# Kernel optimization log

Measured on AMD Instinct MI355X. Metric: run time of the kernel, lower is better.

Reference implementation:

```python
import jax, jax.numpy as jnp
import numpy as np

B, S, D = 2, 2048, 1024
H, DH = 16, 64
E, K, FH = 8, 2, 4096
AUX_W = 0.01
EPS = 1e-6


def setup_inputs() -> dict:
    key = jax.random.key(0)
    ks = jax.random.split(key, 20)
    init = lambda k, shape: (jax.random.normal(k, shape, dtype=jnp.float32) * 0.02)
    return {
        'x': jax.random.normal(ks[0], (B, S, D), dtype=jnp.float32),
        'ln1_s': jnp.ones((D,), jnp.float32), 'ln1_b': jnp.zeros((D,), jnp.float32),
        'Wq': init(ks[1], (D, H * DH)), 'bq': jnp.zeros((H * DH,), jnp.float32),
        'Wk': init(ks[2], (D, H * DH)), 'bk': jnp.zeros((H * DH,), jnp.float32),
        'Wv': init(ks[3], (D, H * DH)), 'bv': jnp.zeros((H * DH,), jnp.float32),
        'Wo': init(ks[4], (H * DH, D)), 'bo': jnp.zeros((D,), jnp.float32),
        'ln2_s': jnp.ones((D,), jnp.float32), 'ln2_b': jnp.zeros((D,), jnp.float32),
        'Wg': init(ks[5], (D, E)), 'bg': jnp.zeros((E,), jnp.float32),
        'W1': init(ks[6], (E, D, FH)), 'b1': jnp.zeros((E, FH), jnp.float32),
        'W2': init(ks[7], (E, FH, D)), 'b2': jnp.zeros((E, D), jnp.float32),
    }


def _layer_norm(x, scale, bias):
    mu = jnp.mean(x, axis=-1, keepdims=True)
    var = jnp.mean(jnp.square(x - mu), axis=-1, keepdims=True)
    return (x - mu) * jax.lax.rsqrt(var + EPS) * scale + bias


def _causal_attn(x, Wq, bq, Wk, bk, Wv, bv, Wo, bo):
    b, s, _ = x.shape
    q = (x @ Wq + bq).reshape(b, s, H, DH)
    k = (x @ Wk + bk).reshape(b, s, H, DH)
    v = (x @ Wv + bv).reshape(b, s, H, DH)
    scores = jnp.einsum('bqhd,bkhd->bhqk', q, k) / jnp.sqrt(jnp.float32(DH))
    causal = jnp.tril(jnp.ones((s, s), dtype=bool))
    scores = jnp.where(causal, scores, jnp.finfo(scores.dtype).min)
    attn = jax.nn.softmax(scores, axis=-1)
    out = jnp.einsum('bhqk,bkhd->bqhd', attn, v).reshape(b, s, H * DH)
    return out @ Wo + bo


def _moe(x, Wg, bg, W1, b1, W2, b2):
    # x: (B,S,D) -> tokens (T,D)
    T = x.shape[0] * x.shape[1]
    xf = x.reshape(T, D)
    logits = xf @ Wg + bg                      # (T,E)
    probs = jax.nn.softmax(logits, axis=-1)
    topv, topi = jax.lax.top_k(probs, K)       # (T,K)
    topv = topv / jnp.sum(topv, axis=-1, keepdims=True)
    combine = jnp.zeros((T, E), xf.dtype).at[jnp.arange(T)[:, None], topi].set(topv)
    out = jnp.zeros((T, D), xf.dtype)
    for e in range(E):  # fixed small expert loop
        h = jax.nn.gelu(xf @ W1[e] + b1[e])
        out = out + combine[:, e:e + 1] * (h @ W2[e] + b2[e])
    # load-balance aux loss
    frac = jnp.mean((combine > 0).astype(jnp.float32), axis=0)
    pmean = jnp.mean(probs, axis=0)
    aux = AUX_W * E * jnp.sum(frac * pmean)
    return out.reshape(x.shape), aux


def reference(x, ln1_s, ln1_b, Wq, bq, Wk, bk, Wv, bv, Wo, bo,
              ln2_s, ln2_b, Wg, bg, W1, b1, W2, b2):
    working = x
    attn_in = _layer_norm(working, ln1_s, ln1_b)
    attn_out = _causal_attn(attn_in, Wq, bq, Wk, bk, Wv, bv, Wo, bo)
    working = working + attn_out
    ffn_in = _layer_norm(working, ln2_s, ln2_b)
    ffn_out, aux = _moe(ffn_in, Wg, bg, W1, b1, W2, b2)
    output = working + ffn_out
    return output, aux
```

## Files before the change

### kernel.cpp

```cpp
#include <hip/hip_runtime.h>
#include <hip/hip_bf16.h>
#include <math.h>

#define Bb 2
#define Ss 2048
#define Dd 1024
#define Hh 16
#define DH 64
#define Ee 8
#define FH 4096
#define Tt (Bb*Ss)

typedef __attribute__((ext_vector_type(8))) short short8;
typedef __attribute__((ext_vector_type(4))) short short4v;
typedef __attribute__((ext_vector_type(4))) float float4v;

#define AS 40

static __device__ inline short f2bf(float f) {
    __hip_bfloat16 h = __float2bfloat16(f);
    return *reinterpret_cast<short*>(&h);
}

__global__ __launch_bounds__(256) void ln_kernel(const float* __restrict__ x,
                                                 const float* __restrict__ sc,
                                                 const float* __restrict__ bi,
                                                 __hip_bfloat16* __restrict__ y) {
    int t = blockIdx.x, tid = threadIdx.x;
    const float* xr = x + (size_t)t * Dd;
    float s1 = 0.f, s2 = 0.f;
    for (int d = tid; d < Dd; d += 256) { float v = xr[d]; s1 += v; s2 += v * v; }
    __shared__ float r1[256], r2[256];
    r1[tid] = s1; r2[tid] = s2; __syncthreads();
    for (int off = 128; off > 0; off >>= 1) {
        if (tid < off) { r1[tid] += r1[tid + off]; r2[tid] += r2[tid + off]; }
        __syncthreads();
    }
    float mu = r1[0] * (1.f / Dd);
    float var = r2[0] * (1.f / Dd) - mu * mu;
    float rstd = rsqrtf(var + 1e-6f);
    __hip_bfloat16* yr = y + (size_t)t * Dd;
    for (int d = tid; d < Dd; d += 256) {
        float v = xr[d];
        yr[d] = __float2bfloat16((v - mu) * rstd * sc[d] + bi[d]);
    }
}

__global__ __launch_bounds__(256) void transpose_qkvo(
    const float* W0, const float* W1, const float* W2, const float* W3,
    __hip_bfloat16* T0, __hip_bfloat16* T1, __hip_bfloat16* T2, __hip_bfloat16* T3) {
    int z = blockIdx.z;
    const float* W = (z == 0) ? W0 : (z == 1) ? W1 : (z == 2) ? W2 : W3;
    __hip_bfloat16* Wt = (z == 0) ? T0 : (z == 1) ? T1 : (z == 2) ? T2 : T3;
    __shared__ float tile[32][33];
    int k0 = blockIdx.y * 32, n0 = blockIdx.x * 32;
    int tx = threadIdx.x & 31, ty = threadIdx.x >> 5;
    #pragma unroll
    for (int p = 0; p < 4; p++)
        tile[ty + p * 8][tx] = W[(size_t)(k0 + ty + p * 8) * Dd + n0 + tx];
    __syncthreads();
    #pragma unroll
    for (int p = 0; p < 4; p++)
        Wt[(size_t)(n0 + ty + p * 8) * Dd + k0 + tx] = __float2bfloat16(tile[tx][ty + p * 8]);
}

__global__ __launch_bounds__(256) void transpose_we(const float* __restrict__ W,
                                                    __hip_bfloat16* __restrict__ Wt,
                                                    int Kd, int N) {
    int e = blockIdx.z;
    W  += (size_t)e * Kd * N;
    Wt += (size_t)e * Kd * N;
    __shared__ float tile[32][33];
    int k0 = blockIdx.y * 32, n0 = blockIdx.x * 32;
    int tx = threadIdx.x & 31, ty = threadIdx.x >> 5;
    #pragma unroll
    for (int p = 0; p < 4; p++)
        tile[ty + p * 8][tx] = W[(size_t)(k0 + ty + p * 8) * N + n0 + tx];
    __syncthreads();
    #pragma unroll
    for (int p = 0; p < 4; p++)
        Wt[(size_t)(n0 + ty + p * 8) * Kd + k0 + tx] = __float2bfloat16(tile[tx][ty + p * 8]);
}

template<int MODE>
__global__ __launch_bounds__(256) void gemm_mfma(
    const __hip_bfloat16* __restrict__ A, const __hip_bfloat16* __restrict__ Bt,
    const float* __restrict__ bias, void* __restrict__ Cv,
    int M, int N, int Kd,
    const int* __restrict__ bucket, const int* __restrict__ cnts,
    const int* __restrict__ bases, const float* __restrict__ residual)
{
    int Me = M;
    const int* rowIdx = nullptr;
    int hbase = 0;
    if (MODE == 2 || MODE == 3) {
        int e = blockIdx.z;
        Me = cnts[e];
        hbase = bases[e];
        Bt += (size_t)e * N * Kd;
        bias += (size_t)e * N;
        if (MODE == 2) rowIdx = bucket + e * Tt;
        if (MODE == 3) A += (size_t)hbase * Kd;
    }
    int m0 = blockIdx.y * 128;
    if (m0 >= Me) return;
    int n0 = blockIdx.x * 128;

    __shared__ __hip_bfloat16 As[128 * AS];
    __shared__ __hip_bfloat16 Bs[128 * AS];

    int tid = threadIdx.x;
    int lane = tid & 63, wave = tid >> 6;
    int wm = (wave & 1) * 64, wn = (wave >> 1) * 64;
    int quad = lane >> 4, l16 = lane & 15;
    int srow = tid >> 2;
    int skg = (tid & 3) * 8;

    float4v acc[4][4];
    #pragma unroll
    for (int i = 0; i < 4; i++)
        #pragma unroll
        for (int j = 0; j < 4; j++) acc[i][j] = (float4v)0.f;

    for (int k0 = 0; k0 < Kd; k0 += 32) {
        #pragma unroll
        for (int p = 0; p < 2; p++) {
            int r = srow + p * 64;
            int gm = m0 + r;
            short8 va = (short8)0;
            if (gm < Me) {
                int row = (MODE == 2) ? rowIdx[gm] : gm;
                va = *(const short8*)(A + (size_t)row * Kd + k0 + skg);
            }
            *(short8*)(&As[r * AS + skg]) = va;
            short8 vb = *(const short8*)(Bt + (size_t)(n0 + r) * Kd + k0 + skg);
            *(short8*)(&Bs[r * AS + skg]) = vb;
        }
        __syncthreads();
        short8 af[4], bf[4];
        #pragma unroll
        for (int i = 0; i < 4; i++)
            af[i] = *(const short8*)(&As[(wm + i * 16 + l16) * AS + quad * 8]);
        #pragma unroll
        for (int j = 0; j < 4; j++)
            bf[j] = *(const short8*)(&Bs[(wn + j * 16 + l16) * AS + quad * 8]);
        #pragma unroll
        for (int i = 0; i < 4; i++)
            #pragma unroll
            for (int j = 0; j < 4; j++)
                acc[i][j] = __builtin_amdgcn_mfma_f32_16x16x32_bf16(af[i], bf[j], acc[i][j], 0, 0, 0);
        __syncthreads();
    }

    #pragma unroll
    for (int i = 0; i < 4; i++) {
        #pragma unroll
        for (int j = 0; j < 4; j++) {
            int col = n0 + wn + j * 16 + l16;
            float bsv = bias[col];
            if (MODE == 4) {
                int mb = m0 + wm + i * 16 + quad * 4;
                int b = mb >> 11, s0 = mb & (Ss - 1);
                int h = col >> 6, d = col & (DH - 1);
                short4v pk;
                #pragma unroll
                for (int r = 0; r < 4; r++) pk[r] = f2bf(acc[i][j][r] + bsv);
                *(short4v*)((__hip_bfloat16*)Cv + ((size_t)(b * Hh + h) * DH + d) * Ss + s0) = pk;
                continue;
            }
            #pragma unroll
            for (int r = 0; r < 4; r++) {
                int m = m0 + wm + i * 16 + quad * 4 + r;
                if (m >= Me) continue;
                float val = acc[i][j][r] + bsv;
                if (MODE == 0) {
                    ((__hip_bfloat16*)Cv)[(size_t)m * N + col] = __float2bfloat16(val);
                } else if (MODE == 1) {
                    ((float*)Cv)[(size_t)m * N + col] = val + residual[(size_t)m * N + col];
                } else if (MODE == 2) {
                    float th = tanhf(0.7978845608028654f * (val + 0.044715f * val * val * val));
                    ((__hip_bfloat16*)Cv)[(size_t)(hbase + m) * N + col] =
                        __float2bfloat16(0.5f * val * (1.f + th));
                } else {
                    ((float*)Cv)[(size_t)(hbase + m) * N + col] = val;
                }
            }
        }
    }
}

__global__ __launch_bounds__(256) void attn_mfma(const __hip_bfloat16* __restrict__ q,
                                                 const __hip_bfloat16* __restrict__ k,
                                                 const __hip_bfloat16* __restrict__ Vt,
                                                 __hip_bfloat16* __restrict__ out) {
    int h = blockIdx.x, tile = blockIdx.y, b = blockIdx.z;
    int wave = threadIdx.x >> 6, lane = threadIdx.x & 63;
    int quad = lane >> 4, l16 = lane & 15;
    int q0 = tile * 64 + wave * 16;
    int tb = b * Ss;

    __shared__ __hip_bfloat16 Ks[32 * 72];
    __shared__ __hip_bfloat16 Vs[64 * 40];

    const __hip_bfloat16* qp = q + (size_t)(tb + q0 + l16) * (Hh * DH) + h * DH + quad * 8;
    short8 qf0 = *(const short8*)(qp);
    short8 qf1 = *(const short8*)(qp + 32);

    float4v oc[4];
    #pragma unroll
    for (int i = 0; i < 4; i++) oc[i] = (float4v)0.f;
    float lsum = 0.f;

    const __hip_bfloat16* kbase = k + (size_t)tb * (Hh * DH) + h * DH;
    const __hip_bfloat16* vbase = Vt + ((size_t)(b * Hh + h) * DH) * Ss;
    int qglob = q0 + l16;
    int srcA = (quad & 1) * 32 + l16;
    int srcB = srcA + 16;
    int sel = quad >> 1;
    int nsteps = 2 * tile + 2;

    int krow = threadIdx.x >> 3, kg = threadIdx.x & 7;
    int vd   = threadIdx.x >> 2, vg = threadIdx.x & 3;

    short8 kv = *(const short8*)(kbase + (size_t)krow * (Hh * DH) + kg * 8);
    short8 vv = *(const short8*)(vbase + (size_t)vd * Ss + vg * 8);

    for (int st = 0; st < nsteps; st++) {
        int k0 = st * 32;
        *(short8*)(&Ks[krow * 72 + kg * 8]) = kv;
        *(short8*)(&Vs[vd * 40 + vg * 8]) = vv;
        __syncthreads();
        if (st + 1 < nsteps) {
            kv = *(const short8*)(kbase + (size_t)(k0 + 32 + krow) * (Hh * DH) + kg * 8);
            vv = *(const short8*)(vbase + (size_t)vd * Ss + (k0 + 32) + vg * 8);
        }

        short8 a0 = *(const short8*)(&Ks[l16 * 72 + quad * 8]);
        short8 a1 = *(const short8*)(&Ks[l16 * 72 + 32 + quad * 8]);
        short8 a2 = *(const short8*)(&Ks[(l16 + 16) * 72 + quad * 8]);
        short8 a3 = *(const short8*)(&Ks[(l16 + 16) * 72 + 32 + quad * 8]);

        float4v c0 = (float4v)0.f, c1 = (float4v)0.f;
        c0 = __builtin_amdgcn_mfma_f32_16x16x32_bf16(a0, qf0, c0, 0, 0, 0);
        c0 = __builtin_amdgcn_mfma_f32_16x16x32_bf16(a1, qf1, c0, 0, 0, 0);
        c1 = __builtin_amdgcn_mfma_f32_16x16x32_bf16(a2, qf0, c1, 0, 0, 0);
        c1 = __builtin_amdgcn_mfma_f32_16x16x32_bf16(a3, qf1, c1, 0, 0, 0);

        float p0[4], p1[4];
        #pragma unroll
        for (int r = 0; r < 4; r++) {
            int key0 = k0 + quad * 4 + r;
            int key1 = key0 + 16;
            p0[r] = (key0 <= qglob) ? __expf(c0[r] * 0.125f - 4.f) : 0.f;
            p1[r] = (key1 <= qglob) ? __expf(c1[r] * 0.125f - 4.f) : 0.f;
            lsum += p0[r] + p1[r];
        }

        short8 pf;
        #pragma unroll
        for (int r = 0; r < 4; r++) {
            float t0 = __shfl(p0[r], srcA), t1 = __shfl(p1[r], srcA);
            pf[r] = f2bf(sel ? t1 : t0);
            float u0 = __shfl(p0[r], srcB), u1 = __shfl(p1[r], srcB);
            pf[4 + r] = f2bf(sel ? u1 : u0);
        }

        #pragma unroll
        for (int nt = 0; nt < 4; nt++) {
            short8 bv = *(const short8*)(&Vs[(nt * 16 + l16) * 40 + quad * 8]);
            oc[nt] = __builtin_amdgcn_mfma_f32_16x16x32_bf16(pf, bv, oc[nt], 0, 0, 0);
        }
        __syncthreads();
    }

    lsum += __shfl_xor(lsum, 16);
    lsum += __shfl_xor(lsum, 32);
    float linv[4];
    #pragma unroll
    for (int r = 0; r < 4; r++) linv[r] = 1.f / __shfl(lsum, quad * 4 + r);

    #pragma unroll
    for (int nt = 0; nt < 4; nt++) {
        #pragma unroll
        for (int r = 0; r < 4; r++) {
            int tokq = tb + q0 + quad * 4 + r;
            out[(size_t)tokq * (Hh * DH) + h * DH + nt * 16 + l16] =
                __float2bfloat16(oc[nt][r] * linv[r]);
        }
    }
}

#define GT 64
__global__ __launch_bounds__(256) void gate_kernel(const float* __restrict__ wk,
                                                   const float* __restrict__ g2s,
                                                   const float* __restrict__ g2b,
                                                   const float* __restrict__ Wg,
                                                   const float* __restrict__ bg,
                                                   float* __restrict__ psum,
                                                   int* __restrict__ counts,
                                                   int* __restrict__ bucket,
                                                   int* __restrict__ eidx,
                                                   int* __restrict__ epos,
                                                   float* __restrict__ ew) {
    int t0 = blockIdx.x * GT;
    int wave = threadIdx.x >> 6, lane = threadIdx.x & 63;

    __shared__ float sp[GT][Ee];
    __shared__ int   sel_e[2][GT];
    __shared__ int   spos[2][GT];
    __shared__ int   lbase[Ee];

    for (int i = wave; i < GT; i += 4) {
        int t = t0 + i;
        const float* xr = wk + (size_t)t * Dd;
        float xv[16];
        float s1 = 0.f, sq = 0.f;
        #pragma unroll
        for (int j = 0; j < 16; j++) {
            float v = xr[lane + j * 64];
            xv[j] = v; s1 += v; sq += v * v;
        }
        #pragma unroll
        for (int off = 32; off; off >>= 1) { s1 += __shfl_xor(s1, off); sq += __shfl_xor(sq, off); }
        float mu = s1 * (1.f / Dd), var = sq * (1.f / Dd) - mu * mu;
        float rstd = rsqrtf(var + 1e-6f);
        float acc[Ee] = {};
        #pragma unroll
        for (int j = 0; j < 16; j++) {
            int d = lane + j * 64;
            float xn = (xv[j] - mu) * rstd * g2s[d] + g2b[d];
            const float* wr = Wg + d * Ee;
            #pragma unroll
            for (int e = 0; e < Ee; e++) acc[e] += xn * wr[e];
        }
        #pragma unroll
        for (int e = 0; e < Ee; e++)
            #pragma unroll
            for (int off = 32; off; off >>= 1) acc[e] += __shfl_xor(acc[e], off);
        if (lane == 0) {
            float lg[Ee], mx = -1e30f;
            #pragma unroll
            for (int e = 0; e < Ee; e++) { lg[e] = acc[e] + bg[e]; mx = fmaxf(mx, lg[e]); }
            float p[Ee], ssum = 0.f;
            #pragma unroll
            for (int e = 0; e < Ee; e++) { p[e] = __expf(lg[e] - mx); ssum += p[e]; }
            float ise = 1.f / ssum;
            #pragma unroll
            for (int e = 0; e < Ee; e++) { p[e] *= ise; sp[i][e] = p[e]; }
            int e1 = 0;
            for (int e = 1; e < Ee; e++) if (p[e] > p[e1]) e1 = e;
            int e2 = -1;
            for (int e = 0; e < Ee; e++) if (e != e1 && (e2 < 0 || p[e] > p[e2])) e2 = e;
            sel_e[0][i] = e1; sel_e[1][i] = e2;
            float w1 = p[e1], w2 = p[e2], isw = 1.f / (w1 + w2);
            eidx[2 * t] = e1; ew[2 * t] = w1 * isw;
            eidx[2 * t + 1] = e2; ew[2 * t + 1] = w2 * isw;
        }
    }
    __syncthreads();

    if (threadIdx.x < Ee) {
        int e = threadIdx.x;
        int local = 0;
        for (int i = 0; i < GT; i++) {
            if (sel_e[0][i] == e) spos[0][i] = local++;
            if (sel_e[1][i] == e) spos[1][i] = local++;
        }
        lbase[e] = atomicAdd(&counts[e], local);
        float ps = 0.f;
        for (int i = 0; i < GT; i++) ps += sp[i][e];
        atomicAdd(&psum[e], ps);
    }
    __syncthreads();

    if (threadIdx.x < GT) {
        int i = threadIdx.x, t = t0 + i;
        #pragma unroll
        for (int s = 0; s < 2; s++) {
            int e = sel_e[s][i];
            int pos = lbase[e] + spos[s][i];
            bucket[e * Tt + pos] = t;
            epos[2 * t + s] = pos;
        }
    }
}

__global__ void zero_init(float* psum, int* counts) {
    int i = threadIdx.x;
    if (i < Ee) { psum[i] = 0.f; counts[i] = 0; }
}

__global__ void prefix_kernel(const int* counts, int* bases) {
    if (threadIdx.x == 0) {
        int run = 0;
        for (int e = 0; e < Ee; e++) { bases[e] = run; run += counts[e]; }
    }
}

__global__ __launch_bounds__(256) void combine_out(const float* __restrict__ working,
                                                   const float* __restrict__ O2,
                                                   const int* __restrict__ bases,
                                                   const int* __restrict__ eidx,
                                                   const int* __restrict__ epos,
                                                   const float* __restrict__ ew,
                                                   float* __restrict__ out) {
    int t = blockIdx.x, tid = threadIdx.x;
    int e0 = eidx[2 * t], e1 = eidx[2 * t + 1];
    size_t r0 = (size_t)(bases[e0] + epos[2 * t]) * Dd;
    size_t r1 = (size_t)(bases[e1] + epos[2 * t + 1]) * Dd;
    float w0 = ew[2 * t], w1 = ew[2 * t + 1];
    const float4* wr = (const float4*)(working + (size_t)t * Dd);
    const float4* o0 = (const float4*)(O2 + r0);
    const float4* o1 = (const float4*)(O2 + r1);
    float4* dst = (float4*)(out + (size_t)t * Dd);
    float4 a = wr[tid], x0 = o0[tid], x1 = o1[tid];
    dst[tid] = make_float4(a.x + w0 * x0.x + w1 * x1.x,
                           a.y + w0 * x0.y + w1 * x1.y,
                           a.z + w0 * x0.z + w1 * x1.z,
                           a.w + w0 * x0.w + w1 * x1.w);
}

__global__ void aux_kernel(const int* counts, const float* psum, float* out) {
    if (threadIdx.x == 0 && blockIdx.x == 0) {
        float a = 0.f;
        for (int e = 0; e < Ee; e++)
            a += (counts[e] * (1.f / Tt)) * (psum[e] * (1.f / Tt));
        out[0] = 0.01f * (float)Ee * a;
    }
}

extern "C" void kernel_launch(void* const* d_in, const int* in_sizes, int n_in,
                              void* d_out, int out_size, void* d_ws, size_t ws_size,
                              hipStream_t stream) {
    const float* x     = (const float*)d_in[0];
    const float* ln1_s = (const float*)d_in[1];
    const float* ln1_b = (const float*)d_in[2];
    const float* Wq    = (const float*)d_in[3];
    const float* bq    = (const float*)d_in[4];
    const float* Wk    = (const float*)d_in[5];
    const float* bk    = (const float*)d_in[6];
    const float* Wv    = (const float*)d_in[7];
    const float* bv    = (const float*)d_in[8];
    const float* Wo    = (const float*)d_in[9];
    const float* bo    = (const float*)d_in[10];
    const float* ln2_s = (const float*)d_in[11];
    const float* ln2_b = (const float*)d_in[12];
    const float* Wg    = (const float*)d_in[13];
    const float* bg    = (const float*)d_in[14];
    const float* W1    = (const float*)d_in[15];
    const float* b1    = (const float*)d_in[16];
    const float* W2    = (const float*)d_in[17];
    const float* b2    = (const float*)d_in[18];

    const size_t MBy = 1u << 20;
    char* base = (char*)d_ws;
    __hip_bfloat16* attn_in = (__hip_bfloat16*)(base);
    __hip_bfloat16* qbf     = (__hip_bfloat16*)(base + 8 * MBy);
    __hip_bfloat16* kbf     = (__hip_bfloat16*)(base + 16 * MBy);
    __hip_bfloat16* Vt      = (__hip_bfloat16*)(base + 24 * MBy);
    float*          working = (float*)(base + 32 * MBy);
    __hip_bfloat16* ffn_in  = (__hip_bfloat16*)(base + 48 * MBy);
    __hip_bfloat16* Hbuf    = (__hip_bfloat16*)(base + 56 * MBy);
    float*          O2      = (float*)(base);
    __hip_bfloat16* WT      = (__hip_bfloat16*)(base + 120 * MBy);
    __hip_bfloat16* WqT     = (__hip_bfloat16*)(base + 120 * MBy);
    __hip_bfloat16* WkT     = (__hip_bfloat16*)(base + 122 * MBy);
    __hip_bfloat16* WvT     = (__hip_bfloat16*)(base + 124 * MBy);
    __hip_bfloat16* WoT     = (__hip_bfloat16*)(base + 126 * MBy);
    char* rt = base + 184 * MBy;
    int*   bucket = (int*)rt;
    int*   counts = (int*)(rt + Ee * Tt * 4);
    int*   bases  = counts + 64;
    float* psum   = (float*)(bases + 64);
    int*   eidx   = (int*)(psum + 64);
    int*   epos   = eidx + 2 * Tt;
    float* ew     = (float*)(epos + 2 * Tt);

    float* out  = (float*)d_out;
    float* auxp = out + (size_t)Tt * Dd;

    zero_init<<<1, 64, 0, stream>>>(psum, counts);
    transpose_qkvo<<<dim3(32, 32, 4), 256, 0, stream>>>(Wq, Wk, Wv, Wo, WqT, WkT, WvT, WoT);
    ln_kernel<<<Tt, 256, 0, stream>>>(x, ln1_s, ln1_b, attn_in);

    dim3 gqkv(Dd / 128, Tt / 128);
    gemm_mfma<0><<<gqkv, 256, 0, stream>>>(attn_in, WqT, bq, qbf, Tt, Dd, Dd,
                                           nullptr, nullptr, nullptr, nullptr);
    gemm_mfma<0><<<gqkv, 256, 0, stream>>>(attn_in, WkT, bk, kbf, Tt, Dd, Dd,
                                           nullptr, nullptr, nullptr, nullptr);
    gemm_mfma<4><<<gqkv, 256, 0, stream>>>(attn_in, WvT, bv, Vt, Tt, Dd, Dd,
                                           nullptr, nullptr, nullptr, nullptr);

    attn_mfma<<<dim3(Hh, Ss / 64, Bb), 256, 0, stream>>>(qbf, kbf, Vt, attn_in);

    gemm_mfma<1><<<gqkv, 256, 0, stream>>>(attn_in, WoT, bo, working, Tt, Dd, Dd,
                                           nullptr, nullptr, nullptr, x);

    ln_kernel<<<Tt, 256, 0, stream>>>(working, ln2_s, ln2_b, ffn_in);
    gate_kernel<<<Tt / GT, 256, 0, stream>>>(working, ln2_s, ln2_b, Wg, bg,
                                             psum, counts, bucket, eidx, epos, ew);
    prefix_kernel<<<1, 64, 0, stream>>>(counts, bases);

    transpose_we<<<dim3(FH / 32, Dd / 32, Ee), 256, 0, stream>>>(W1, WT, Dd, FH);
    gemm_mfma<2><<<dim3(FH / 128, Tt / 128, Ee), 256, 0, stream>>>(
        ffn_in, WT, b1, Hbuf, Tt, FH, Dd, bucket, counts, bases, nullptr);
    transpose_we<<<dim3(Dd / 32, FH / 32, Ee), 256, 0, stream>>>(W2, WT, FH, Dd);
    gemm_mfma<3><<<dim3(Dd / 128, Tt / 128, Ee), 256, 0, stream>>>(
        Hbuf, WT, b2, O2, Tt, Dd, FH, bucket, counts, bases, nullptr);

    combine_out<<<Tt, 256, 0, stream>>>(working, O2, bases, eidx, epos, ew, out);
    aux_kernel<<<1, 64, 0, stream>>>(counts, psum, auxp);
}
```

Measured before the change: 1.004 ms.

## Load GEMM tiles directly to LDS with global_load_lds and XOR swizzle

Replaces the register-staged global-to-shared tile loads in the generic GEMM with direct global_load_lds 16-byte transfers, and drops the padded shared-memory row stride in favour of an XOR-swizzled 32-wide layout to avoid bank conflicts. This removes the VGPR round trip and per-iteration address and bounds computation, precomputing the gathered row pointers once. Rows past the expert count now load row 0 (MODE 2) or read out of range instead of zero-filling, so correctness relies on the epilogue masking those rows. There is also no wait on the asynchronous loads before the barrier beyond what the compiler inserts.

```diff
diff --git a/kernel.cpp b/kernel.cpp
--- a/kernel.cpp
+++ b/kernel.cpp
@@ -15,11 +15,15 @@
 typedef __attribute__((ext_vector_type(4))) short short4v;
 typedef __attribute__((ext_vector_type(4))) float float4v;
 
-#define AS 40
-
 static __device__ inline short f2bf(float f) {
     __hip_bfloat16 h = __float2bfloat16(f);
     return *reinterpret_cast<short*>(&h);
+}
+
+static __device__ inline void glds16(const __hip_bfloat16* g, __hip_bfloat16* l) {
+    __builtin_amdgcn_global_load_lds(
+        (const __attribute__((address_space(1))) unsigned int*)g,
+        (__attribute__((address_space(3))) unsigned int*)l, 16, 0, 0);
 }
 
 __global__ __launch_bounds__(256) void ln_kernel(const float* __restrict__ x,
@@ -106,15 +110,39 @@
     if (m0 >= Me) return;
     int n0 = blockIdx.x * 128;
 
-    __shared__ __hip_bfloat16 As[128 * AS];
-    __shared__ __hip_bfloat16 Bs[128 * AS];
+    __shared__ __hip_bfloat16 As[128 * 32];
+    __shared__ __hip_bfloat16 Bs[128 * 32];
 
     int tid = threadIdx.x;
     int lane = tid & 63, wave = tid >> 6;
     int wm = (wave & 1) * 64, wn = (wave >> 1) * 64;
     int quad = lane >> 4, l16 = lane & 15;
-    int srow = tid >> 2;
-    int skg = (tid & 3) * 8;
+
+    int rs = lane >> 2;
+    int sslot = (lane & 3) ^ ((lane >> 3) & 3);
+    int rowS0 = 16 * (2 * wave + 0) + rs;
+    int rowS1 = 16 * (2 * wave + 1) + rs;
+
+    const __hip_bfloat16 *gA0, *gA1;
+    if (MODE == 2) {
+        int g0 = m0 + rowS0, g1 = m0 + rowS1;
+        int r0 = (g0 < Me) ? rowIdx[g0] : 0;
+        int r1 = (g1 < Me) ? rowIdx[g1] : 0;
+        gA0 = A + (size_t)r0 * Kd + sslot * 8;
+        gA1 = A + (size_t)r1 * Kd + sslot * 8;
+    } else {
+        gA0 = A + (size_t)(m0 + rowS0) * Kd + sslot * 8;
+        gA1 = A + (size_t)(m0 + rowS1) * Kd + sslot * 8;
+    }
+    const __hip_bfloat16* gB0 = Bt + (size_t)(n0 + rowS0) * Kd + sslot * 8;
+    const __hip_bfloat16* gB1 = Bt + (size_t)(n0 + rowS1) * Kd + sslot * 8;
+
+    __hip_bfloat16* lA0 = As + (2 * wave + 0) * 512;
+    __hip_bfloat16* lA1 = As + (2 * wave + 1) * 512;
+    __hip_bfloat16* lB0 = Bs + (2 * wave + 0) * 512;
+    __hip_bfloat16* lB1 = Bs + (2 * wave + 1) * 512;
+
+    int rsw = (l16 >> 1) & 3;
 
     float4v acc[4][4];
     #pragma unroll
@@ -123,27 +151,18 @@
         for (int j = 0; j < 4; j++) acc[i][j] = (float4v)0.f;
 
     for (int k0 = 0; k0 < Kd; k0 += 32) {
-        #pragma unroll
-        for (int p = 0; p < 2; p++) {
-            int r = srow + p * 64;
-            int gm = m0 + r;
-            short8 va = (short8)0;
-            if (gm < Me) {
-                int row = (MODE == 2) ? rowIdx[gm] : gm;
-                va = *(const short8*)(A + (size_t)row * Kd + k0 + skg);
-            }
-            *(short8*)(&As[r * AS + skg]) = va;
-            short8 vb = *(const short8*)(Bt + (size_t)(n0 + r) * Kd + k0 + skg);
-            *(short8*)(&Bs[r * AS + skg]) = vb;
-        }
+        glds16(gA0 + k0, lA0);
+        glds16(gA1 + k0, lA1);
+        glds16(gB0 + k0, lB0);
+        glds16(gB1 + k0, lB1);
         __syncthreads();
         short8 af[4], bf[4];
         #pragma unroll
         for (int i = 0; i < 4; i++)
-            af[i] = *(const short8*)(&As[(wm + i * 16 + l16) * AS + quad * 8]);
+            af[i] = *(const short8*)(&As[(wm + i * 16 + l16) * 32 + ((quad ^ rsw) * 8)]);
         #pragma unroll
         for (int j = 0; j < 4; j++)
-            bf[j] = *(const short8*)(&Bs[(wn + j * 16 + l16) * AS + quad * 8]);
+            bf[j] = *(const short8*)(&Bs[(wn + j * 16 + l16) * 32 + ((quad ^ rsw) * 8)]);
         #pragma unroll
         for (int i = 0; i < 4; i++)
             #pragma unroll
```

Measured after the change: 927.9 us. -7.6%, faster.
